# Optimization experiments

Hardware: AMD Instinct MI355X
Metric: run time of the kernel (lower is better)

The kernel has to match this reference:

```python
import jax, jax.numpy as jnp
import numpy as np


def setup_inputs() -> dict:
    key = jax.random.key(0)
    ks = iter(jax.random.split(key, 48))
    B, W, L = 256, 128, 3          # bsz, n_walks, walk length (events per walk)
    N, E = 10000, 200000           # num nodes, num edges
    ND = 172                       # node_dim == time_dim (TGAT-style features)
    ED = 172                       # edge_dim
    H = 128                        # hid_dim
    EV = ED + 3 + ND               # event_dim = 347
    D2 = 2 * H                     # attention input_dim = 2*hid_dim
    MD = H + 12                    # mlp_dim (if_cat=True)

    def nrm(shape, s=0.05):
        return jax.random.normal(next(ks), shape, jnp.float32) * s

    inp = {
        # embedding tables
        'node_table': nrm((N, ND), 0.1),
        'edge_table': nrm((E, ED), 0.1),
        # TimeEncode params
        'basis_freq': jnp.asarray(1.0 / 10 ** np.linspace(0, 9, ND), jnp.float32),
        'phase': jnp.zeros((ND,), jnp.float32),
        # event_gcn: lin_event + 2-layer MLP
        'ev_W': nrm((EV, ND)), 'ev_b': jnp.zeros((ND,), jnp.float32),
        'ev_m1W': nrm((ND, H)), 'ev_m1b': jnp.zeros((H,), jnp.float32),
        'ev_m2W': nrm((H, H)), 'ev_m2b': jnp.zeros((H,), jnp.float32),
        # TemporalAwareAttention: W1, W2 (bias init 0.1), 2-layer MLP
        'at_W1': nrm((D2, D2)), 'at_b1': jnp.zeros((D2,), jnp.float32),
        'at_W2': nrm((D2, D2)), 'at_b2': jnp.full((D2,), 0.1, jnp.float32),
        'at_m1W': nrm((D2, H)), 'at_m1b': jnp.zeros((H,), jnp.float32),
        'at_m2W': nrm((H, H)), 'at_m2b': jnp.zeros((H,), jnp.float32),
        # final scoring MLP (mlp_dim -> mlp_dim -> hid -> 1)
        'f_W1': nrm((MD, MD)), 'f_b1': jnp.zeros((MD,), jnp.float32),
        'f_W2': nrm((MD, H)), 'f_b2': jnp.zeros((H,), jnp.float32),
        'f_W3': nrm((H, 1)), 'f_b3': jnp.zeros((1,), jnp.float32),
        # walk data
        'time_idx': jax.random.uniform(next(ks), (B, W, L), jnp.float32) * 1e4,
        'cut_time_l': jax.random.uniform(next(ks), (B,), jnp.float32) * 1e4 + 1e4,
        'cat_feat': nrm((B, W, 12), 1.0),
        'edge_identify': jax.random.uniform(next(ks), (B, W, L, 3), jnp.float32),
        'node_idx': jax.random.randint(next(ks), (B, W, 2 * L), 0, N),
        'edge_idx': jax.random.randint(next(ks), (B, W, L), 0, E),
    }
    return inp


def reference(node_table, edge_table, basis_freq, phase,
              ev_W, ev_b, ev_m1W, ev_m1b, ev_m2W, ev_m2b,
              at_W1, at_b1, at_W2, at_b2, at_m1W, at_m1b, at_m2W, at_m2b,
              f_W1, f_b1, f_W2, f_b2, f_W3, f_b3,
              time_idx, cut_time_l, cat_feat, edge_identify,
              node_idx, edge_idx):
    # ---- feature retrieval ----
    edge_feat = edge_table[edge_idx]                           # [B,W,L,ED]
    delta = cut_time_l[:, None, None] - time_idx               # [B,W,L]
    time_feat = jnp.cos(delta[..., None] * basis_freq + phase) # [B,W,L,ND]
    event = jnp.concatenate([edge_feat, edge_identify, time_feat], axis=-1)  # [B,W,L,347]
    src = node_table[node_idx[:, :, 0::2]]                     # [B,W,L,ND]
    tgt = node_table[node_idx[:, :, 1::2]]                     # [B,W,L,ND]

    # ---- event_gcn (GINEConv-style), applied twice ----
    def conv(s, t):
        ev = event @ ev_W + ev_b
        msg = jax.nn.relu(t + ev)
        h = jax.nn.relu((s + msg) @ ev_m1W + ev_m1b)
        return h @ ev_m2W + ev_m2b                             # [B,W,L,H]

    upd = jnp.concatenate([conv(src, tgt), conv(tgt, src)], axis=-1)  # [B,W,L,2H]

    # ---- temporal-aware attention over walk positions ----
    s_feat = upd[:, :, 2:3, :]                                 # [B,W,1,2H]
    t_feat = upd[:, :, :2, :]                                  # [B,W,2,2H]
    Wp = s_feat @ at_W1 + at_b1
    Wq = t_feat @ at_W2 + at_b2
    scores = jnp.einsum('bwid,bwjd->bwij', Wp, Wq)             # [B,W,1,2]
    diff = jnp.abs(cut_time_l[:, None, None] - time_idx[:, :, :2])
    tw = jnp.exp(-diff / (jnp.std(diff, ddof=1) + 1e-6))       # [B,W,2]
    scores = scores * (0.7 + 0.3 * tw[:, :, None, :])
    alpha = jax.nn.softmax(scores, axis=-1)
    out = s_feat + jnp.einsum('bwij,bwjd->bwid', alpha, Wq)    # residual on raw src
    h = jax.nn.relu(out @ at_m1W + at_m1b)
    h = (h @ at_m2W + at_m2b)[:, :, 0, :]                      # [B,W,H]

    # ---- final per-walk scoring MLP (if_cat: concat 12-d cat features) ----
    x = jnp.concatenate([h, cat_feat], axis=-1)                # [B,W,H+12]
    z = jax.nn.relu(x @ f_W1 + f_b1)
    z = jax.nn.relu(z @ f_W2 + f_b2)
    return z @ f_W3 + f_b3                                     # [B,W,1]
```

## Files before the change

### kernel.cpp

```cpp
#include <hip/hip_runtime.h>
#include <math.h>

#define NWIN_TOTAL (256 * 128)
#define NTH 256
#define CDIV(a, b) (((a) + (b) - 1) / (b))

typedef _Float16 f16x8 __attribute__((ext_vector_type(8)));
typedef float f32x4 __attribute__((ext_vector_type(4)));

__device__ __forceinline__ void mma1(f16x8 a, f16x8 bh, f32x4& c) {
    c = __builtin_amdgcn_mfma_f32_16x16x32_f16(a, bh, c, 0, 0, 0);
}

__global__ __launch_bounds__(NTH) void k_std(const float* __restrict__ time_idx,
                                             const float* __restrict__ cut,
                                             double* __restrict__ acc) {
    int tid = threadIdx.x;
    const int n = NWIN_TOTAL * 2;
    double s = 0.0, s2 = 0.0;
    for (int i = blockIdx.x * blockDim.x + tid; i < n; i += gridDim.x * blockDim.x) {
        int j = i & 1;
        int bw = i >> 1;
        float d = fabsf(cut[bw >> 7] - time_idx[bw * 3 + j]);
        s += (double)d;
        s2 += (double)d * (double)d;
    }
    __shared__ double ls[NTH], ls2[NTH];
    ls[tid] = s; ls2[tid] = s2;
    __syncthreads();
    for (int st = NTH / 2; st > 0; st >>= 1) {
        if (tid < st) { ls[tid] += ls[tid + st]; ls2[tid] += ls2[tid + st]; }
        __syncthreads();
    }
    if (tid == 0) { atomicAdd(&acc[0], ls[0]); atomicAdd(&acc[1], ls2[0]); }
}

struct WEnt { const float* src; _Float16* dH; int Kt, Nt, Kp, Np, off; };
struct WAll { WEnt w[9]; int grand; };

__global__ __launch_bounds__(NTH) void k_wprep_all(WAll a) {
    int idx = blockIdx.x * NTH + threadIdx.x;
    if (idx >= a.grand) return;
    int i = 0;
#pragma unroll
    for (int t = 0; t < 8; ++t)
        if (i + 1 < 9 && idx >= a.w[i + 1].off) ++i;
    const WEnt& e = a.w[i];
    int lidx = idx - e.off;
    int nks = e.Kp / 32;
    int cg = lidx / (nks * 64);
    int rem = lidx - cg * nks * 64;
    int ks = rem >> 6, lane = rem & 63;
    int col = cg * 16 + (lane & 15);
    for (int j = 0; j < 8; ++j) {
        int k = ks * 32 + ((lane >> 4) << 3) + j;
        float v = (k < e.Kt && col < e.Nt) ? e.src[(size_t)k * e.Nt + col] : 0.f;
        e.dH[(size_t)lidx * 8 + j] = (_Float16)v;
    }
}

template <int RG>
__device__ __forceinline__ void frag_store_hf(_Float16* AH, int r, int o,
                                              const float* v) {
    int B = ((o >> 2) * RG + (r >> 4)) * 64 + ((r & 15) | ((o & 3) << 4));
    int off = (B ^ ((B >> 4) & 7)) * 8;
    f16x8 h8;
#pragma unroll
    for (int e = 0; e < 8; ++e) h8[e] = (_Float16)v[e];
    *(f16x8*)&AH[off] = h8;
}

template <int RG>
__device__ __forceinline__ void frag_store_h(_Float16* AH, int r, int o, f16x8 v) {
    int B = ((o >> 2) * RG + (r >> 4)) * 64 + ((r & 15) | ((o & 3) << 4));
    int off = (B ^ ((B >> 4) & 7)) * 8;
    *(f16x8*)&AH[off] = v;
}

template <int RG, int NREP>
__device__ __forceinline__ void mfma_step_h(const _Float16* AH,
                                            const _Float16* __restrict__ Wh,
                                            int nks, int ks, int k2, int wv, int lane,
                                            f32x4 (&acc)[RG][NREP]) {
    f16x8 ah[RG];
#pragma unroll
    for (int rg = 0; rg < RG; ++rg) {
        int B = (k2 * RG + rg) * 64 + lane;
        int off = (B ^ ((B >> 4) & 7)) * 8;
        ah[rg] = *(const f16x8*)&AH[off];
    }
#pragma unroll
    for (int j = 0; j < NREP; ++j) {
        int cg = wv * NREP + j;
        size_t boff = ((size_t)(cg * nks + ks) * 64 + lane) * 8;
        f16x8 bh = *(const f16x8*)&Wh[boff];
#pragma unroll
        for (int rg = 0; rg < RG; ++rg) mma1(ah[rg], bh, acc[rg][j]);
    }
}

struct GCP {
    const _Float16 *W0h, *W1h, *W2h;
    const float *b0, *b1, *b2;
    _Float16* upd; int M; int win0;
    const float* edge_table; const float* node_table;
    const float* basis_freq; const float* phase;
    const float* time_idx; const float* cut;
    const int* edge_idx; const int* node_idx; const float* eid;
};

__global__ __launch_bounds__(NTH) void k_gc(GCP p) {
    __shared__ _Float16 AH[2][2048];
    __shared__ _Float16 evL[32 * 184];
    __shared__ _Float16 h1L[32 * 136];
    __shared__ float ldsBF[176], ldsPH[176];
    const int tid = threadIdx.x, wv = tid >> 6, lane = tid & 63;
    const int mtile = blockIdx.x * 32;
    const int o = tid & 7, r = tid >> 3;

    if (tid < 172) { ldsBF[tid] = p.basis_freq[tid]; ldsPH[tid] = p.phase[tid]; }

    int grow = mtile + r; if (grow >= p.M) grow = p.M - 1;
    int w3 = grow / 3, l = grow - w3 * 3;
    int gw = p.win0 + w3;
    int nb = gw * 6 + 2 * l;
    const float* er = p.edge_table + (size_t)p.edge_idx[gw * 3 + l] * 172;
    const float* S0 = p.node_table + (size_t)p.node_idx[nb] * 172;
    const float* T0 = p.node_table + (size_t)p.node_idx[nb + 1] * 172;
    float dlt = p.cut[gw >> 7] - p.time_idx[gw * 3 + l];
    float g[3][8]; float eidv[3];
#pragma unroll
    for (int kc = 0; kc < 3; ++kc) {
        int k0 = kc * 64 + o * 8;
        if (k0 + 7 < 172) {
            float4 x = *(const float4*)&er[k0];
            float4 y = *(const float4*)&er[k0 + 4];
            g[kc][0]=x.x; g[kc][1]=x.y; g[kc][2]=x.z; g[kc][3]=x.w;
            g[kc][4]=y.x; g[kc][5]=y.y; g[kc][6]=y.z; g[kc][7]=y.w;
        } else if (k0 == 168) {
            float4 x = *(const float4*)&er[168];
            g[kc][0]=x.x; g[kc][1]=x.y; g[kc][2]=x.z; g[kc][3]=x.w;
            eidv[0] = p.eid[(gw * 3 + l) * 3 + 0];
            eidv[1] = p.eid[(gw * 3 + l) * 3 + 1];
            eidv[2] = p.eid[(gw * 3 + l) * 3 + 2];
        }
    }
    __syncthreads();

    {
        f32x4 acc[2][3];
#pragma unroll
        for (int rg = 0; rg < 2; ++rg)
#pragma unroll
            for (int j = 0; j < 3; ++j)
#pragma unroll
                for (int i = 0; i < 4; ++i) acc[rg][j][i] = 0.f;
        const int ord[6] = {3, 4, 5, 0, 1, 2};
#pragma unroll
        for (int x = 0; x < 6; ++x) {
            const int kc = ord[x];
            {
                int k0 = kc * 64 + o * 8;
                float v[8];
                if (kc >= 3 || k0 >= 176) {
#pragma unroll
                    for (int e = 0; e < 8; ++e) {
                        int k = k0 + e;
                        int q = k - 175;
                        v[e] = (k < 347) ? __cosf(fmaf(dlt, ldsBF[q], ldsPH[q])) : 0.f;
                    }
                } else if (k0 + 7 < 172) {
#pragma unroll
                    for (int e = 0; e < 8; ++e) v[e] = g[kc][e];
                } else {
                    v[0]=g[2][0]; v[1]=g[2][1]; v[2]=g[2][2]; v[3]=g[2][3];
                    v[4]=eidv[0]; v[5]=eidv[1]; v[6]=eidv[2];
                    v[7]=__cosf(fmaf(dlt, ldsBF[0], ldsPH[0]));
                }
                frag_store_hf<2>(AH[x & 1], r, o, v);
            }
            __syncthreads();
#pragma unroll
            for (int k2 = 0; k2 < 2; ++k2) {
                if (kc == 5 && k2 == 1) continue;
                mfma_step_h<2, 3>(AH[x & 1], p.W0h, 12,
                                  kc * 2 + k2, k2, wv, lane, acc);
            }
        }
#pragma unroll
        for (int j = 0; j < 3; ++j) {
            int col = (wv * 3 + j) * 16 + (lane & 15);
            if (col < 176) {
                float b = (col < 172) ? p.b0[col] : 0.f;
#pragma unroll
                for (int rg = 0; rg < 2; ++rg)
#pragma unroll
                    for (int i = 0; i < 4; ++i) {
                        int row = rg * 16 + ((lane >> 4) << 2) + i;
                        evL[row * 184 + col] = (_Float16)(acc[rg][j][i] + b);
                    }
            }
        }
    }
    __syncthreads();

    f32x4 a1[2][2][2];
#pragma unroll
    for (int d = 0; d < 2; ++d)
#pragma unroll
        for (int rg = 0; rg < 2; ++rg)
#pragma unroll
            for (int j = 0; j < 2; ++j)
#pragma unroll
                for (int i = 0; i < 4; ++i) a1[d][rg][j][i] = 0.f;
    {
        float Ps[8], Pt[8];
        auto loadST = [&](int kc) {
            int k0 = kc * 64 + o * 8;
            if (k0 + 7 < 172) {
                *(float4*)&Ps[0] = *(const float4*)&S0[k0];
                *(float4*)&Ps[4] = *(const float4*)&S0[k0 + 4];
                *(float4*)&Pt[0] = *(const float4*)&T0[k0];
                *(float4*)&Pt[4] = *(const float4*)&T0[k0 + 4];
            } else if (k0 == 168) {
                *(float4*)&Ps[0] = *(const float4*)&S0[168];
                *(float4*)&Pt[0] = *(const float4*)&T0[168];
            }
        };
        loadST(0);
#pragma unroll
        for (int kc = 0; kc < 3; ++kc) {
            {
                int k0 = kc * 64 + o * 8;
                float v0[8], v1[8];
                if (k0 + 7 < 172) {
                    f16x8 e8 = *(const f16x8*)&evL[r * 184 + k0];
#pragma unroll
                    for (int e = 0; e < 8; ++e) {
                        float ev = (float)e8[e];
                        v0[e] = Ps[e] + fmaxf(Pt[e] + ev, 0.f);
                        v1[e] = Pt[e] + fmaxf(Ps[e] + ev, 0.f);
                    }
                } else if (k0 == 168) {
                    f16x8 e8 = *(const f16x8*)&evL[r * 184 + 168];
#pragma unroll
                    for (int e = 0; e < 8; ++e) {
                        if (e < 4) {
                            float ev = (float)e8[e];
                            v0[e] = Ps[e] + fmaxf(Pt[e] + ev, 0.f);
                            v1[e] = Pt[e] + fmaxf(Ps[e] + ev, 0.f);
                        } else { v0[e] = 0.f; v1[e] = 0.f; }
                    }
                } else {
#pragma unroll
                    for (int e = 0; e < 8; ++e) { v0[e] = 0.f; v1[e] = 0.f; }
                }
                frag_store_hf<2>(AH[0], r, o, v0);
                frag_store_hf<2>(AH[1], r, o, v1);
            }
            if (kc < 2) loadST(kc + 1);
            __syncthreads();
#pragma unroll
            for (int k2 = 0; k2 < 2; ++k2) {
                const int ks = kc * 2 + k2;
                f16x8 ah[2][2];
#pragma unroll
                for (int d = 0; d < 2; ++d)
#pragma unroll
                    for (int rg = 0; rg < 2; ++rg) {
                        int B = (k2 * 2 + rg) * 64 + lane;
                        int off = (B ^ ((B >> 4) & 7)) * 8;
                        ah[d][rg] = *(const f16x8*)&AH[d][off];
                    }
#pragma unroll
                for (int j = 0; j < 2; ++j) {
                    size_t boff = ((size_t)((wv * 2 + j) * 6 + ks) * 64 + lane) * 8;
                    f16x8 bh = *(const f16x8*)&p.W1h[boff];
#pragma unroll
                    for (int d = 0; d < 2; ++d)
#pragma unroll
                        for (int rg = 0; rg < 2; ++rg)
                            mma1(ah[d][rg], bh, a1[d][rg][j]);
                }
            }
            __syncthreads();
        }
    }

    for (int dir = 0; dir < 2; ++dir) {
#pragma unroll
        for (int j = 0; j < 2; ++j) {
            int col = (wv * 2 + j) * 16 + (lane & 15);
            float b = p.b1[col];
#pragma unroll
            for (int rg = 0; rg < 2; ++rg)
#pragma unroll
                for (int i = 0; i < 4; ++i) {
                    int row = rg * 16 + ((lane >> 4) << 2) + i;
                    float x = a1[dir][rg][j][i] + b;
                    h1L[row * 136 + col] = (_Float16)(x > 0.f ? x : 0.f);
                }
        }
        __syncthreads();

        f32x4 a2[2][2];
#pragma unroll
        for (int rg = 0; rg < 2; ++rg)
#pragma unroll
            for (int j = 0; j < 2; ++j)
#pragma unroll
                for (int i = 0; i < 4; ++i) a2[rg][j][i] = 0.f;
#pragma unroll
        for (int ks = 0; ks < 4; ++ks) {
            const int k0 = ks * 32 + ((lane >> 4) << 3);
            f16x8 a4[2];
#pragma unroll
            for (int rg = 0; rg < 2; ++rg)
                a4[rg] = *(const f16x8*)&h1L[(rg * 16 + (lane & 15)) * 136 + k0];
#pragma unroll
            for (int j = 0; j < 2; ++j) {
                size_t boff = ((size_t)((wv * 2 + j) * 4 + ks) * 64 + lane) * 8;
                f16x8 bh = *(const f16x8*)&p.W2h[boff];
#pragma unroll
                for (int rg = 0; rg < 2; ++rg) mma1(a4[rg], bh, a2[rg][j]);
            }
        }
#pragma unroll
        for (int j = 0; j < 2; ++j) {
            int col = (wv * 2 + j) * 16 + (lane & 15);
            float b = p.b2[col];
#pragma unroll
            for (int rg = 0; rg < 2; ++rg)
#pragma unroll
                for (int i = 0; i < 4; ++i) {
                    int row = mtile + rg * 16 + ((lane >> 4) << 2) + i;
                    if (row < p.M)
                        p.upd[(size_t)row * 256 + dir * 128 + col] = (_Float16)(a2[rg][j][i] + b);
                }
        }
        if (dir == 0) __syncthreads();
    }
}

struct AttnP {
    const _Float16* upd;
    const _Float16 *W1h,*W2h,*M1h,*M2h,*F1h,*F2h;
    const float *ab1,*ab2,*am1b,*am2b,*fb1,*fb2,*fW3,*fb3;
    const float *time_idx,*cut,*cat; const double* acc;
    float* out; int nw; int win0;
};

__global__ __launch_bounds__(NTH) void k_attn(AttnP p) {
    __shared__ float R1[32 * 260];
    __shared__ _Float16 R2h[64 * 264];
    __shared__ _Float16 AH2[2][2048];
    __shared__ float scoreL[64], aL[64], finL[32];
    float* R2f = (float*)R2h;
    const int tid = threadIdx.x, wv = tid >> 6, lane = tid & 63;
    const int w0 = blockIdx.x * 32;
    const int rr = tid >> 3, o = tid & 7;
    if (tid < 64) scoreL[tid] = 0.f;
    if (tid < 32) finL[tid] = 0.f;
    __syncthreads();

    {
        int lw = w0 + rr; if (lw >= p.nw) lw = p.nw - 1;
        const _Float16* Ar = p.upd + ((size_t)lw * 3 + 2) * 256;
        f32x4 acc[2][4];
#pragma unroll
        for (int rg = 0; rg < 2; ++rg)
#pragma unroll
            for (int j = 0; j < 4; ++j)
#pragma unroll
                for (int i = 0; i < 4; ++i) acc[rg][j][i] = 0.f;
        f16x8 P = *(const f16x8*)&Ar[o * 8];
#pragma unroll
        for (int kc = 0; kc < 4; ++kc) {
            frag_store_h<2>(AH2[kc & 1], rr, o, P);
            if (kc < 3) P = *(const f16x8*)&Ar[(kc + 1) * 64 + o * 8];
            __syncthreads();
#pragma unroll
            for (int k2 = 0; k2 < 2; ++k2)
                mfma_step_h<2, 4>(AH2[kc & 1], p.W1h, 8, kc * 2 + k2, k2, wv, lane, acc);
        }
#pragma unroll
        for (int j = 0; j < 4; ++j) {
            int col = (wv * 4 + j) * 16 + (lane & 15);
            float b = p.ab1[col];
#pragma unroll
            for (int rg = 0; rg < 2; ++rg)
#pragma unroll
                for (int i = 0; i < 4; ++i) {
                    int row = rg * 16 + ((lane >> 4) << 2) + i;
                    R1[row * 260 + col] = acc[rg][j][i] + b;
                }
        }
    }

    for (int st = 0; st < 2; ++st) {
        int g = st * 32 + rr;
        int lw = w0 + (g >> 1); if (lw >= p.nw) lw = p.nw - 1;
        const _Float16* Ar = p.upd + ((size_t)lw * 3 + (g & 1)) * 256;
        f32x4 acc[2][4];
#pragma unroll
        for (int rg = 0; rg < 2; ++rg)
#pragma unroll
            for (int j = 0; j < 4; ++j)
#pragma unroll
                for (int i = 0; i < 4; ++i) acc[rg][j][i] = 0.f;
        f16x8 P = *(const f16x8*)&Ar[o * 8];
#pragma unroll
        for (int kc = 0; kc < 4; ++kc) {
            frag_store_h<2>(AH2[kc & 1], rr, o, P);
            if (kc < 3) P = *(const f16x8*)&Ar[(kc + 1) * 64 + o * 8];
            __syncthreads();
#pragma unroll
            for (int k2 = 0; k2 < 2; ++k2)
                mfma_step_h<2, 4>(AH2[kc & 1], p.W2h, 8, kc * 2 + k2, k2, wv, lane, acc);
        }
        float scp[2][4];
#pragma unroll
        for (int rg = 0; rg < 2; ++rg)
#pragma unroll
            for (int i = 0; i < 4; ++i) scp[rg][i] = 0.f;
#pragma unroll
        for (int j = 0; j < 4; ++j) {
            int col = (wv * 4 + j) * 16 + (lane & 15);
            float b = p.ab2[col];
#pragma unroll
            for (int rg = 0; rg < 2; ++rg)
#pragma unroll
                for (int i = 0; i < 4; ++i) {
                    int row = rg * 16 + ((lane >> 4) << 2) + i;
                    int gg = st * 32 + row;
                    float v = acc[rg][j][i] + b;
                    R2h[gg * 264 + col] = (_Float16)v;
                    scp[rg][i] += v * R1[(gg >> 1) * 260 + col];
                }
        }
#pragma unroll
        for (int rg = 0; rg < 2; ++rg)
#pragma unroll
            for (int i = 0; i < 4; ++i) {
                float sv = scp[rg][i];
#pragma unroll
                for (int off = 1; off < 16; off <<= 1) sv += __shfl_xor(sv, off);
                if ((lane & 15) == 0) {
                    int gg = st * 32 + rg * 16 + ((lane >> 4) << 2) + i;
                    atomicAdd(&scoreL[gg], sv);
                }
            }
    }
    __syncthreads();

    if (tid < 32) {
        int lw = w0 + tid; if (lw >= p.nw) lw = p.nw - 1;
        int gw = p.win0 + lw;
        const double n = (double)(NWIN_TOTAL * 2);
        float stdv = (float)sqrt((p.acc[1] - p.acc[0] * p.acc[0] / n) / (n - 1.0));
        float cutv = p.cut[gw >> 7];
        float d0 = fabsf(cutv - p.time_idx[gw * 3 + 0]);
        float d1 = fabsf(cutv - p.time_idx[gw * 3 + 1]);
        float tw0 = expf(-d0 / (stdv + 1e-6f));
        float tw1 = expf(-d1 / (stdv + 1e-6f));
        float s0 = scoreL[tid * 2 + 0] * (0.7f + 0.3f * tw0);
        float s1 = scoreL[tid * 2 + 1] * (0.7f + 0.3f * tw1);
        float m = fmaxf(s0, s1);
        float e0 = expf(s0 - m), e1 = expf(s1 - m);
        float inv = 1.f / (e0 + e1);
        aL[tid * 2 + 0] = e0 * inv;
        aL[tid * 2 + 1] = e1 * inv;
    }
    __syncthreads();

    {
        int lw = w0 + rr; if (lw >= p.nw) lw = p.nw - 1;
        const _Float16* U2 = p.upd + ((size_t)lw * 3 + 2) * 256;
        f32x4 acc[2][2];
#pragma unroll
        for (int rg = 0; rg < 2; ++rg)
#pragma unroll
            for (int j = 0; j < 2; ++j)
#pragma unroll
                for (int i = 0; i < 4; ++i) acc[rg][j][i] = 0.f;
        for (int kc = 0; kc < 4; ++kc) {
            __syncthreads();
            {
                int k0 = kc * 64 + o * 8;
                float a0 = aL[rr * 2], a1v = aL[rr * 2 + 1];
                f16x8 u8 = *(const f16x8*)&U2[k0];
                f16x8 q0 = *(const f16x8*)&R2h[(rr * 2) * 264 + k0];
                f16x8 q1 = *(const f16x8*)&R2h[(rr * 2 + 1) * 264 + k0];
                float v[8];
#pragma unroll
                for (int e = 0; e < 8; ++e)
                    v[e] = (float)u8[e] + a0 * (float)q0[e] + a1v * (float)q1[e];
                frag_store_hf<2>(AH2[0], rr, o, v);
            }
            __syncthreads();
#pragma unroll
            for (int k2 = 0; k2 < 2; ++k2)
                mfma_step_h<2, 2>(AH2[0], p.M1h, 8, kc * 2 + k2, k2, wv, lane, acc);
        }
        __syncthreads();
#pragma unroll
        for (int j = 0; j < 2; ++j) {
            int col = (wv * 2 + j) * 16 + (lane & 15);
            float b = p.am1b[col];
#pragma unroll
            for (int rg = 0; rg < 2; ++rg)
#pragma unroll
                for (int i = 0; i < 4; ++i) {
                    int row = rg * 16 + ((lane >> 4) << 2) + i;
                    float x = acc[rg][j][i] + b;
                    R2f[row * 132 + col] = x > 0.f ? x : 0.f;
                }
        }
    }
    __syncthreads();

    for (int q = tid; q < 32 * 68; q += NTH) {
        int r = q / 68, c = 128 + q % 68;
        int lw = w0 + r; if (lw >= p.nw) lw = p.nw - 1;
        int gw = p.win0 + lw;
        R1[r * 196 + c] = (c < 140) ? p.cat[(size_t)gw * 12 + (c - 128)] : 0.f;
    }

    {
        f32x4 acc[2][2];
#pragma unroll
        for (int rg = 0; rg < 2; ++rg)
#pragma unroll
            for (int j = 0; j < 2; ++j)
#pragma unroll
                for (int i = 0; i < 4; ++i) acc[rg][j][i] = 0.f;
        for (int kc = 0; kc < 2; ++kc) {
            __syncthreads();
            {
                int k0 = kc * 64 + o * 8;
                float v[8];
                float4 x = *(const float4*)&R2f[rr * 132 + k0];
                float4 y = *(const float4*)&R2f[rr * 132 + k0 + 4];
                v[0]=x.x; v[1]=x.y; v[2]=x.z; v[3]=x.w;
                v[4]=y.x; v[5]=y.y; v[6]=y.z; v[7]=y.w;
                frag_store_hf<2>(AH2[0], rr, o, v);
            }
            __syncthreads();
#pragma unroll
            for (int k2 = 0; k2 < 2; ++k2)
                mfma_step_h<2, 2>(AH2[0], p.M2h, 4, kc * 2 + k2, k2, wv, lane, acc);
        }
        __syncthreads();
#pragma unroll
        for (int j = 0; j < 2; ++j) {
            int col = (wv * 2 + j) * 16 + (lane & 15);
            float b = p.am2b[col];
#pragma unroll
            for (int rg = 0; rg < 2; ++rg)
#pragma unroll
                for (int i = 0; i < 4; ++i) {
                    int row = rg * 16 + ((lane >> 4) << 2) + i;
                    R1[row * 196 + col] = acc[rg][j][i] + b;
                }
        }
    }

    {
        f32x4 acc[2][3];
#pragma unroll
        for (int rg = 0; rg < 2; ++rg)
#pragma unroll
            for (int j = 0; j < 3; ++j)
#pragma unroll
                for (int i = 0; i < 4; ++i) acc[rg][j][i] = 0.f;
        for (int kc = 0; kc < 3; ++kc) {
            __syncthreads();
            {
                int k0 = kc * 64 + o * 8;
                float v[8];
                float4 x = *(const float4*)&R1[rr * 196 + k0];
                float4 y = *(const float4*)&R1[rr * 196 + k0 + 4];
                v[0]=x.x; v[1]=x.y; v[2]=x.z; v[3]=x.w;
                v[4]=y.x; v[5]=y.y; v[6]=y.z; v[7]=y.w;
                frag_store_hf<2>(AH2[0], rr, o, v);
            }
            __syncthreads();
#pragma unroll
            for (int k2 = 0; k2 < 2; ++k2)
                mfma_step_h<2, 3>(AH2[0], p.F1h, 6, kc * 2 + k2, k2, wv, lane, acc);
        }
        __syncthreads();
#pragma unroll
        for (int j = 0; j < 3; ++j) {
            int col = (wv * 3 + j) * 16 + (lane & 15);
            float b = (col < 140) ? p.fb1[col] : 0.f;
#pragma unroll
            for (int rg = 0; rg < 2; ++rg)
#pragma unroll
                for (int i = 0; i < 4; ++i) {
                    int row = rg * 16 + ((lane >> 4) << 2) + i;
                    float x = acc[rg][j][i] + b;
                    R2f[row * 196 + col] = x > 0.f ? x : 0.f;
                }
        }
    }

    {
        f32x4 acc[2][2];
#pragma unroll
        for (int rg = 0; rg < 2; ++rg)
#pragma unroll
            for (int j = 0; j < 2; ++j)
#pragma unroll
                for (int i = 0; i < 4; ++i) acc[rg][j][i] = 0.f;
        for (int kc = 0; kc < 3; ++kc) {
            __syncthreads();
            {
                int k0 = kc * 64 + o * 8;
                float v[8];
                float4 x = *(const float4*)&R2f[rr * 196 + k0];
                float4 y = *(const float4*)&R2f[rr * 196 + k0 + 4];
                v[0]=x.x; v[1]=x.y; v[2]=x.z; v[3]=x.w;
                v[4]=y.x; v[5]=y.y; v[6]=y.z; v[7]=y.w;
                frag_store_hf<2>(AH2[0], rr, o, v);
            }
            __syncthreads();
#pragma unroll
            for (int k2 = 0; k2 < 2; ++k2)
                mfma_step_h<2, 2>(AH2[0], p.F2h, 6, kc * 2 + k2, k2, wv, lane, acc);
        }
        float pt[2][4];
#pragma unroll
        for (int rg = 0; rg < 2; ++rg)
#pragma unroll
            for (int i = 0; i < 4; ++i) pt[rg][i] = 0.f;
#pragma unroll
        for (int j = 0; j < 2; ++j) {
            int col = (wv * 2 + j) * 16 + (lane & 15);
            float b = p.fb2[col];
            float w3 = p.fW3[col];
#pragma unroll
            for (int rg = 0; rg < 2; ++rg)
#pragma unroll
                for (int i = 0; i < 4; ++i) {
                    float x = acc[rg][j][i] + b;
                    x = x > 0.f ? x : 0.f;
                    pt[rg][i] += x * w3;
                }
        }
#pragma unroll
        for (int rg = 0; rg < 2; ++rg)
#pragma unroll
            for (int i = 0; i < 4; ++i) {
                float sv = pt[rg][i];
#pragma unroll
                for (int off = 1; off < 16; off <<= 1) sv += __shfl_xor(sv, off);
                if ((lane & 15) == 0)
                    atomicAdd(&finL[rg * 16 + ((lane >> 4) << 2) + i], sv);
            }
    }
    __syncthreads();
    if (tid < 32 && w0 + tid < p.nw)
        p.out[p.win0 + w0 + tid] = finL[tid] + p.fb3[0];
}

extern "C" void kernel_launch(void* const* d_in, const int* in_sizes, int n_in,
                              void* d_out, int out_size, void* d_ws, size_t ws_size,
                              hipStream_t stream) {
    const float* node_table    = (const float*)d_in[0];
    const float* edge_table    = (const float*)d_in[1];
    const float* basis_freq    = (const float*)d_in[2];
    const float* phase         = (const float*)d_in[3];
    const float* ev_W          = (const float*)d_in[4];
    const float* ev_b          = (const float*)d_in[5];
    const float* ev_m1W        = (const float*)d_in[6];
    const float* ev_m1b        = (const float*)d_in[7];
    const float* ev_m2W        = (const float*)d_in[8];
    const float* ev_m2b        = (const float*)d_in[9];
    const float* at_W1         = (const float*)d_in[10];
    const float* at_b1         = (const float*)d_in[11];
    const float* at_W2         = (const float*)d_in[12];
    const float* at_b2         = (const float*)d_in[13];
    const float* at_m1W        = (const float*)d_in[14];
    const float* at_m1b        = (const float*)d_in[15];
    const float* at_m2W        = (const float*)d_in[16];
    const float* at_m2b        = (const float*)d_in[17];
    const float* f_W1          = (const float*)d_in[18];
    const float* f_b1          = (const float*)d_in[19];
    const float* f_W2          = (const float*)d_in[20];
    const float* f_b2          = (const float*)d_in[21];
    const float* f_W3          = (const float*)d_in[22];
    const float* f_b3          = (const float*)d_in[23];
    const float* time_idx      = (const float*)d_in[24];
    const float* cut_time_l    = (const float*)d_in[25];
    const float* cat_feat      = (const float*)d_in[26];
    const float* edge_identify = (const float*)d_in[27];
    const int*   node_idx      = (const int*)d_in[28];
    const int*   edge_idx      = (const int*)d_in[29];

    char* wsb = (char*)d_ws;
    double* acc = (double*)wsb;

    const int   wkp[9] = {384, 192, 128, 256, 256, 256, 128, 192, 192};
    const int   wnp[9] = {192, 128, 128, 256, 256, 128, 128, 192, 128};
    const int   wkt[9] = {347, 172, 128, 256, 256, 256, 128, 140, 140};
    const int   wnt[9] = {172, 128, 128, 256, 256, 128, 128, 140, 128};
    const float* wsrc[9] = {ev_W, ev_m1W, ev_m2W, at_W1, at_W2, at_m1W, at_m2W, f_W1, f_W2};
    _Float16* wH[9];
    size_t woff = 256;
    WAll wa = {};
    int cum = 0;
    for (int i = 0; i < 9; ++i) {
        size_t plane = (size_t)wkp[i] * wnp[i];
        wH[i] = (_Float16*)(wsb + woff);
        woff += plane * sizeof(_Float16);
        woff = (woff + 15) & ~(size_t)15;
        wa.w[i].src = wsrc[i]; wa.w[i].dH = wH[i];
        wa.w[i].Kt = wkt[i]; wa.w[i].Nt = wnt[i]; wa.w[i].Kp = wkp[i]; wa.w[i].Np = wnp[i];
        wa.w[i].off = cum;
        cum += (wnp[i] / 16) * (wkp[i] / 32) * 64;
    }
    wa.grand = cum;

    hipMemsetAsync(d_ws, 0, 16, stream);
    k_std<<<64, NTH, 0, stream>>>(time_idx, cut_time_l, acc);
    k_wprep_all<<<CDIV(wa.grand, NTH), NTH, 0, stream>>>(wa);

    size_t avail = ws_size > woff + 4096 ? ws_size - woff - 4096 : 0;
    size_t nwc_s = avail / 1536;
    int nwc = (int)(nwc_s > NWIN_TOTAL ? NWIN_TOTAL : nwc_s);
    if (nwc < 1) nwc = 1;
    _Float16* updB = (_Float16*)(wsb + ((woff + 255) & ~(size_t)255));

    for (int c0 = 0; c0 < NWIN_TOTAL; c0 += nwc) {
        int nw = NWIN_TOTAL - c0 < nwc ? NWIN_TOTAL - c0 : nwc;
        int M3 = nw * 3;

        GCP gc = {};
        gc.W0h = wH[0]; gc.W1h = wH[1]; gc.W2h = wH[2];
        gc.b0 = ev_b; gc.b1 = ev_m1b; gc.b2 = ev_m2b;
        gc.upd = updB; gc.M = M3; gc.win0 = c0;
        gc.edge_table = edge_table; gc.node_table = node_table;
        gc.basis_freq = basis_freq; gc.phase = phase;
        gc.time_idx = time_idx; gc.cut = cut_time_l;
        gc.edge_idx = edge_idx; gc.node_idx = node_idx; gc.eid = edge_identify;
        k_gc<<<CDIV(M3, 32), NTH, 0, stream>>>(gc);

        AttnP ap = {};
        ap.upd = updB;
        ap.W1h = wH[3]; ap.W2h = wH[4];
        ap.M1h = wH[5]; ap.M2h = wH[6];
        ap.F1h = wH[7]; ap.F2h = wH[8];
        ap.ab1 = at_b1; ap.ab2 = at_b2; ap.am1b = at_m1b; ap.am2b = at_m2b;
        ap.fb1 = f_b1; ap.fb2 = f_b2; ap.fW3 = f_W3; ap.fb3 = f_b3;
        ap.time_idx = time_idx; ap.cut = cut_time_l; ap.cat = cat_feat; ap.acc = acc;
        ap.out = (float*)d_out; ap.nw = nw; ap.win0 = c0;
        k_attn<<<CDIV(nw, 32), NTH, 0, stream>>>(ap);
    }
}
```

Measured before the change: 157.0 us.

## Store MLP activations as fp16 row-major LDS and feed MFMA directly

The tail MLP layers of the attention kernel now write their intermediate activations to shared memory as fp16 in a row-major layout. The next layer's MFMA reads its A fragments straight from that buffer, which removes the per-chunk repack into AH2 and the two barriers around each repack. The cat-feature fill is moved earlier, alongside the softmax, and goes directly into the fp16 input buffer. Intermediates are rounded to fp16 earlier than before, and LDS reads with strides of 136 and 200 halves may cause bank conflicts.

```diff
diff --git a/kernel.cpp b/kernel.cpp
--- a/kernel.cpp
+++ b/kernel.cpp
@@ -355,7 +355,9 @@
     __shared__ _Float16 R2h[64 * 264];
     __shared__ _Float16 AH2[2][2048];
     __shared__ float scoreL[64], aL[64], finL[32];
-    float* R2f = (float*)R2h;
+    _Float16* H2L = (_Float16*)R1;
+    _Float16* XZL = ((_Float16*)R1) + 8192;
+    _Float16* Z1L = (_Float16*)R1;
     const int tid = threadIdx.x, wv = tid >> 6, lane = tid & 63;
     const int w0 = blockIdx.x * 32;
     const int rr = tid >> 3, o = tid & 7;
@@ -471,6 +473,13 @@
         aL[tid * 2 + 0] = e0 * inv;
         aL[tid * 2 + 1] = e1 * inv;
     }
+    for (int q = tid; q < 32 * 72; q += NTH) {
+        int r2 = q / 72, c = 128 + q % 72;
+        int lw = w0 + r2; if (lw >= p.nw) lw = p.nw - 1;
+        int gw = p.win0 + lw;
+        XZL[r2 * 200 + c] = (c < 140) ? (_Float16)p.cat[(size_t)gw * 12 + (c - 128)]
+                                      : (_Float16)0.f;
+    }
     __syncthreads();
 
     {
@@ -513,18 +522,11 @@
                 for (int i = 0; i < 4; ++i) {
                     int row = rg * 16 + ((lane >> 4) << 2) + i;
                     float x = acc[rg][j][i] + b;
-                    R2f[row * 132 + col] = x > 0.f ? x : 0.f;
-                }
-        }
-    }
-    __syncthreads();
-
-    for (int q = tid; q < 32 * 68; q += NTH) {
-        int r = q / 68, c = 128 + q % 68;
-        int lw = w0 + r; if (lw >= p.nw) lw = p.nw - 1;
-        int gw = p.win0 + lw;
-        R1[r * 196 + c] = (c < 140) ? p.cat[(size_t)gw * 12 + (c - 128)] : 0.f;
-    }
+                    H2L[row * 136 + col] = (_Float16)(x > 0.f ? x : 0.f);
+                }
+        }
+    }
+    __syncthreads();
 
     {
         f32x4 acc[2][2];
@@ -534,23 +536,21 @@
             for (int j = 0; j < 2; ++j)
 #pragma unroll
                 for (int i = 0; i < 4; ++i) acc[rg][j][i] = 0.f;
-        for (int kc = 0; kc < 2; ++kc) {
-            __syncthreads();
-            {
-                int k0 = kc * 64 + o * 8;
-                float v[8];
-                float4 x = *(const float4*)&R2f[rr * 132 + k0];
-                float4 y = *(const float4*)&R2f[rr * 132 + k0 + 4];
-                v[0]=x.x; v[1]=x.y; v[2]=x.z; v[3]=x.w;
-                v[4]=y.x; v[5]=y.y; v[6]=y.z; v[7]=y.w;
-                frag_store_hf<2>(AH2[0], rr, o, v);
-            }
-            __syncthreads();
-#pragma unroll
-            for (int k2 = 0; k2 < 2; ++k2)
-                mfma_step_h<2, 2>(AH2[0], p.M2h, 4, kc * 2 + k2, k2, wv, lane, acc);
-        }
-        __syncthreads();
+#pragma unroll
+        for (int ks = 0; ks < 4; ++ks) {
+            const int k0 = ks * 32 + ((lane >> 4) << 3);
+            f16x8 a4[2];
+#pragma unroll
+            for (int rg = 0; rg < 2; ++rg)
+                a4[rg] = *(const f16x8*)&H2L[(rg * 16 + (lane & 15)) * 136 + k0];
+#pragma unroll
+            for (int j = 0; j < 2; ++j) {
+                size_t boff = ((size_t)((wv * 2 + j) * 4 + ks) * 64 + lane) * 8;
+                f16x8 bh = *(const f16x8*)&p.M2h[boff];
+#pragma unroll
+                for (int rg = 0; rg < 2; ++rg) mma1(a4[rg], bh, acc[rg][j]);
+            }
+        }
 #pragma unroll
         for (int j = 0; j < 2; ++j) {
             int col = (wv * 2 + j) * 16 + (lane & 15);
@@ -560,10 +560,11 @@
 #pragma unroll
                 for (int i = 0; i < 4; ++i) {
                     int row = rg * 16 + ((lane >> 4) << 2) + i;
-                    R1[row * 196 + col] = acc[rg][j][i] + b;
-                }
-        }
-    }
+                    XZL[row * 200 + col] = (_Float16)(acc[rg][j][i] + b);
+                }
+        }
+    }
+    __syncthreads();
 
     {
         f32x4 acc[2][3];
@@ -573,21 +574,20 @@
             for (int j = 0; j < 3; ++j)
 #pragma unroll
                 for (int i = 0; i < 4; ++i) acc[rg][j][i] = 0.f;
-        for (int kc = 0; kc < 3; ++kc) {
-            __syncthreads();
-            {
-                int k0 = kc * 64 + o * 8;
-                float v[8];
-                float4 x = *(const float4*)&R1[rr * 196 + k0];
-                float4 y = *(const float4*)&R1[rr * 196 + k0 + 4];
-                v[0]=x.x; v[1]=x.y; v[2]=x.z; v[3]=x.w;
-                v[4]=y.x; v[5]=y.y; v[6]=y.z; v[7]=y.w;
-                frag_store_hf<2>(AH2[0], rr, o, v);
-            }
-            __syncthreads();
-#pragma unroll
-            for (int k2 = 0; k2 < 2; ++k2)
-                mfma_step_h<2, 3>(AH2[0], p.F1h, 6, kc * 2 + k2, k2, wv, lane, acc);
+#pragma unroll
+        for (int ks = 0; ks < 6; ++ks) {
+            const int k0 = ks * 32 + ((lane >> 4) << 3);
+            f16x8 a4[2];
+#pragma unroll
+            for (int rg = 0; rg < 2; ++rg)
+                a4[rg] = *(const f16x8*)&XZL[(rg * 16 + (lane & 15)) * 200 + k0];
+#pragma unroll
+            for (int j = 0; j < 3; ++j) {
+                size_t boff = ((size_t)((wv * 3 + j) * 6 + ks) * 64 + lane) * 8;
+                f16x8 bh = *(const f16x8*)&p.F1h[boff];
+#pragma unroll
+                for (int rg = 0; rg < 2; ++rg) mma1(a4[rg], bh, acc[rg][j]);
+            }
         }
         __syncthreads();
 #pragma unroll
@@ -600,10 +600,11 @@
                 for (int i = 0; i < 4; ++i) {
                     int row = rg * 16 + ((lane >> 4) << 2) + i;
                     float x = acc[rg][j][i] + b;
-                    R2f[row * 196 + col] = x > 0.f ? x : 0.f;
-                }
-        }
-    }
+                    Z1L[row * 200 + col] = (_Float16)(x > 0.f ? x : 0.f);
+                }
+        }
+    }
+    __syncthreads();
 
     {
         f32x4 acc[2][2];
@@ -613,21 +614,20 @@
             for (int j = 0; j < 2; ++j)
 #pragma unroll
                 for (int i = 0; i < 4; ++i) acc[rg][j][i] = 0.f;
-        for (int kc = 0; kc < 3; ++kc) {
-            __syncthreads();
-            {
-                int k0 = kc * 64 + o * 8;
-                float v[8];
-                float4 x = *(const float4*)&R2f[rr * 196 + k0];
-                float4 y = *(const float4*)&R2f[rr * 196 + k0 + 4];
-                v[0]=x.x; v[1]=x.y; v[2]=x.z; v[3]=x.w;
-                v[4]=y.x; v[5]=y.y; v[6]=y.z; v[7]=y.w;
-                frag_store_hf<2>(AH2[0], rr, o, v);
-            }
-            __syncthreads();
-#pragma unroll
-            for (int k2 = 0; k2 < 2; ++k2)
-                mfma_step_h<2, 2>(AH2[0], p.F2h, 6, kc * 2 + k2, k2, wv, lane, acc);
+#pragma unroll
+        for (int ks = 0; ks < 6; ++ks) {
+            const int k0 = ks * 32 + ((lane >> 4) << 3);
+            f16x8 a4[2];
+#pragma unroll
+            for (int rg = 0; rg < 2; ++rg)
+                a4[rg] = *(const f16x8*)&Z1L[(rg * 16 + (lane & 15)) * 200 + k0];
+#pragma unroll
+            for (int j = 0; j < 2; ++j) {
+                size_t boff = ((size_t)((wv * 2 + j) * 6 + ks) * 64 + lane) * 8;
+                f16x8 bh = *(const f16x8*)&p.F2h[boff];
+#pragma unroll
+                for (int rg = 0; rg < 2; ++rg) mma1(a4[rg], bh, acc[rg][j]);
+            }
         }
         float pt[2][4];
 #pragma unroll
```

New measurement: 156.1 us. About the same (-0.6%).
